# Kernel optimization log

Hardware: AMD Instinct MI355X
Metric: run time of the kernel (lower is better)

## Reference

```python
import jax, jax.numpy as jnp
import numpy as np

B, S, D = 4, 2048, 1024
H = 16
HD = D // H  # head dim = 64


def setup_inputs() -> dict:
    key = jax.random.key(0)
    ks = jax.random.split(key, 9)
    sc = 1.0 / np.sqrt(D)
    return {
        "x": jax.random.normal(ks[0], (B, S, D), jnp.float32),
        "Wq_w": jax.random.normal(ks[1], (D, D), jnp.float32) * sc,
        "Wq_b": jax.random.normal(ks[2], (D,), jnp.float32) * 0.01,
        "Wk_w": jax.random.normal(ks[3], (D, D), jnp.float32) * sc,
        "Wk_b": jax.random.normal(ks[4], (D,), jnp.float32) * 0.01,
        "Wv_w": jax.random.normal(ks[5], (D, D), jnp.float32) * sc,
        "Wv_b": jax.random.normal(ks[6], (D,), jnp.float32) * 0.01,
        "Wo_w": jax.random.normal(ks[7], (D, D), jnp.float32) * sc,
        "Wo_b": jax.random.normal(ks[8], (D,), jnp.float32) * 0.01,
    }


def reference(x, Wq_w, Wq_b, Wk_w, Wk_b, Wv_w, Wv_b, Wo_w, Wo_b):
    b, s, _ = x.shape
    # QKV projections (weights stored [in, out])
    q = x @ Wq_w + Wq_b
    k = x @ Wk_w + Wk_b
    v = x @ Wv_w + Wv_b
    # [b, s, D] -> [b, H, s, hd]
    q = q.reshape(b, s, H, HD).transpose(0, 2, 1, 3)
    k = k.reshape(b, s, H, HD).transpose(0, 2, 1, 3)
    v = v.reshape(b, s, H, HD).transpose(0, 2, 1, 3)
    # naive attention: full [b, H, s, s] scores, scale by head_dim**0.5
    scores = jnp.einsum("bhqd,bhkd->bhqk", q, k) / jnp.sqrt(jnp.float32(HD))
    # faithful to torch: tril(scores)==0 -> -inf (causal mask via tril of values)
    filt = jnp.tril(scores)
    scores = jnp.where(filt == 0, jnp.float32(-jnp.inf), scores)
    probs = jax.nn.softmax(scores, axis=-1)
    attn = jnp.einsum("bhqk,bhkd->bhqd", probs, v)
    # [b, H, s, hd] -> [b, s, D]
    attn = attn.transpose(0, 2, 1, 3).reshape(b, s, D)
    return attn @ Wo_w + Wo_b
```

## Files before the change

### kernel.cpp

```cpp
#include <hip/hip_runtime.h>
#include <hip/hip_bf16.h>


#define B_  4
#define S_  2048
#define D_  1024
#define H_  16
#define HD_ 64
#define M_  (B_*S_)
#define NT_ (S_/64)

typedef unsigned short u16;
typedef __attribute__((ext_vector_type(8))) short bf16x8;
typedef __attribute__((ext_vector_type(4))) float f32x4;
typedef __attribute__((ext_vector_type(8))) unsigned short ush8;
typedef __attribute__((ext_vector_type(4))) unsigned short ush4;

static __device__ __forceinline__ u16 f2b(float f) {
    unsigned int u = __float_as_uint(f);
    return (u16)((u + 0x7fffu + ((u >> 16) & 1u)) >> 16);
}

static __device__ __forceinline__ int cvt_pk_bf16(float a, float b) {
    int r;
    asm("v_cvt_pk_bf16_f32 %0, %1, %2" : "=v"(r) : "v"(a), "v"(b));
    return r;
}

#define EXP2(x) exp2f(x)

#define GLOAD_LDS16(g, l)                                                      \
    __builtin_amdgcn_global_load_lds(                                          \
        (const __attribute__((address_space(1))) void*)(g),                    \
        (__attribute__((address_space(3))) void*)(l), 16, 0, 0)

__global__ __launch_bounds__(256)
void cast_f32_bf16(const float* __restrict__ in, u16* __restrict__ out, int n8)
{
    int i = blockIdx.x * blockDim.x + threadIdx.x;
    const int stride = gridDim.x * blockDim.x;
    for (; i < n8; i += stride) {
        const float4 a = ((const float4*)in)[i*2+0];
        const float4 b = ((const float4*)in)[i*2+1];
        ush8 o;
        o[0]=f2b(a.x); o[1]=f2b(a.y); o[2]=f2b(a.z); o[3]=f2b(a.w);
        o[4]=f2b(b.x); o[5]=f2b(b.y); o[6]=f2b(b.z); o[7]=f2b(b.w);
        ((ush8*)out)[i] = o;
    }
}

__global__ __launch_bounds__(256)
void transpose_cast(const float* __restrict__ W, u16* __restrict__ Wt)
{
    __shared__ u16 T[64*72];
    const int tid = threadIdx.x;
    const int k0 = blockIdx.x * 64, n0 = blockIdx.y * 64;
    #pragma unroll
    for (int it = 0; it < 4; ++it) {
        const int li = tid + it*256;
        const int kk = li >> 4;
        const int nc = (li & 15) * 4;
        const float4 w4 = *(const float4*)&W[(size_t)(k0+kk)*D_ + n0 + nc];
        T[(nc+0)*72 + kk] = f2b(w4.x);
        T[(nc+1)*72 + kk] = f2b(w4.y);
        T[(nc+2)*72 + kk] = f2b(w4.z);
        T[(nc+3)*72 + kk] = f2b(w4.w);
    }
    __syncthreads();
    #pragma unroll
    for (int it = 0; it < 2; ++it) {
        const int li = tid + it*256;
        const int nr = li >> 3;
        const int kc = (li & 7) * 8;
        const ush8 v = *(const ush8*)&T[nr*72 + kc];
        *(ush8*)&Wt[(size_t)(n0+nr)*D_ + k0 + kc] = v;
    }
}

#define QSCALE 0.18033688f
#define TP_ 136

__global__ __launch_bounds__(256)
void gemm_qkv(const u16* __restrict__ A,
              const u16* __restrict__ wq, const u16* __restrict__ wk,
              const u16* __restrict__ wv,
              const float* __restrict__ bq, const float* __restrict__ bk,
              const float* __restrict__ bv,
              u16* __restrict__ oq, u16* __restrict__ ok, u16* __restrict__ ovt)
{
    __shared__ u16 sh[64*TP_];
    u16* As = sh;
    u16* Bs = sh + 4096;

    const int tid  = threadIdx.x;
    const int lane = tid & 63;
    const int wave = tid >> 6;
    const int wr = wave >> 1, wc = wave & 1;
    const int bm = blockIdx.x * 128;
    const int sel = blockIdx.y >> 3;
    const int bn = (blockIdx.y & 7) * 128;
    const u16* Bt = sel == 0 ? wq : sel == 1 ? wk : wv;
    const float* bias = sel == 0 ? bq : sel == 1 ? bk : bv;

    const int srow = wave*32 + (lane >> 2);
    const int sk   = (lane & 3) * 8;
    const u16* gA0 = A  + (size_t)(bm + srow)      * D_ + sk;
    const u16* gA1 = A  + (size_t)(bm + srow + 16) * D_ + sk;
    const u16* gB0 = Bt + (size_t)(bn + srow)      * D_ + sk;
    const u16* gB1 = Bt + (size_t)(bn + srow + 16) * D_ + sk;
    u16* lA0 = &As[(wave*2+0)*512];
    u16* lA1 = &As[(wave*2+1)*512];
    u16* lB0 = &Bs[(wave*2+0)*512];
    u16* lB1 = &Bs[(wave*2+1)*512];

    const f32x4 z4 = {0.f, 0.f, 0.f, 0.f};
    f32x4 acc[4][4];
    #pragma unroll
    for (int i = 0; i < 4; ++i)
        #pragma unroll
        for (int j = 0; j < 4; ++j) acc[i][j] = z4;

    const int cl = lane & 15;
    const int g  = lane >> 4;

    for (int k0 = 0; k0 < D_; k0 += 32) {
        GLOAD_LDS16(gA0 + k0, lA0);
        GLOAD_LDS16(gA1 + k0, lA1);
        GLOAD_LDS16(gB0 + k0, lB0);
        GLOAD_LDS16(gB1 + k0, lB1);
        __syncthreads();

        bf16x8 af[4], bfv[4];
        #pragma unroll
        for (int mf = 0; mf < 4; ++mf)
            af[mf] = *(const bf16x8*)&As[(wr*64 + mf*16 + cl)*32 + g*8];
        #pragma unroll
        for (int nf = 0; nf < 4; ++nf)
            bfv[nf] = *(const bf16x8*)&Bs[(wc*64 + nf*16 + cl)*32 + g*8];
        __builtin_amdgcn_s_setprio(1);
        #pragma unroll
        for (int mf = 0; mf < 4; ++mf)
            #pragma unroll
            for (int nf = 0; nf < 4; ++nf)
                acc[mf][nf] = __builtin_amdgcn_mfma_f32_16x16x32_bf16(
                    af[mf], bfv[nf], acc[mf][nf], 0, 0, 0);
        __builtin_amdgcn_s_setprio(0);
        __syncthreads();
    }

    if (sel == 2) {
        const int b = bm >> 11, s0 = bm & (S_-1);
        u16* T = sh;
        #pragma unroll
        for (int hh = 0; hh < 2; ++hh) {
            if (wc == hh) {
                #pragma unroll
                for (int nf = 0; nf < 4; ++nf) {
                    const float bvv = bias[bn + wc*64 + nf*16 + cl];
                    #pragma unroll
                    for (int mf = 0; mf < 4; ++mf) {
                        ush4 o4;
                        #pragma unroll
                        for (int r = 0; r < 4; ++r)
                            o4[r] = f2b(acc[mf][nf][r] + bvv);
                        *(ush4*)&T[(nf*16 + cl)*TP_ + wr*64 + mf*16 + g*4] = o4;
                    }
                }
            }
            __syncthreads();
            const int h = (bn >> 6) + hh;
            #pragma unroll
            for (int pp = 0; pp < 4; ++pp) {
                const int d = wave*16 + pp*4 + g;
                const ush8 vv = *(const ush8*)&T[d*TP_ + cl*8];
                *(ush8*)&ovt[((size_t)((b*H_ + h)*HD_ + d))*S_ + s0 + cl*8] = vv;
            }
            __syncthreads();
        }
    } else {
        const float oscale = sel == 0 ? QSCALE : 1.0f;
        u16* o = sel == 0 ? oq : ok;
        #pragma unroll
        for (int nf = 0; nf < 4; ++nf) {
            const int col = bn + wc*64 + nf*16 + cl;
            const float bvv = bias[col];
            const int h = col >> 6, d = col & (HD_-1);
            #pragma unroll
            for (int mf = 0; mf < 4; ++mf) {
                #pragma unroll
                for (int r = 0; r < 4; ++r) {
                    const int row = bm + wr*64 + mf*16 + g*4 + r;
                    const float v = (acc[mf][nf][r] + bvv) * oscale;
                    const int bb = row >> 11, s = row & (S_-1);
                    o[((size_t)(bb*H_ + h)*S_ + s)*HD_ + d] = f2b(v);
                }
            }
        }
    }
}

__global__ __launch_bounds__(256)
void gemm_oproj(const u16* __restrict__ A, const u16* __restrict__ Bt,
                const float* __restrict__ bias, float* __restrict__ out)
{
    __shared__ u16 As[128*32];
    __shared__ u16 Bs[128*32];
    const int tid  = threadIdx.x;
    const int lane = tid & 63;
    const int wave = tid >> 6;
    const int wr = wave >> 1, wc = wave & 1;
    const int bm = blockIdx.x * 128, bn = blockIdx.y * 128;

    const int srow = wave*32 + (lane >> 2);
    const int sk   = (lane & 3) * 8;
    const u16* gA0 = A  + (size_t)(bm + srow)      * D_ + sk;
    const u16* gA1 = A  + (size_t)(bm + srow + 16) * D_ + sk;
    const u16* gB0 = Bt + (size_t)(bn + srow)      * D_ + sk;
    const u16* gB1 = Bt + (size_t)(bn + srow + 16) * D_ + sk;
    u16* lA0 = &As[(wave*2+0)*512];
    u16* lA1 = &As[(wave*2+1)*512];
    u16* lB0 = &Bs[(wave*2+0)*512];
    u16* lB1 = &Bs[(wave*2+1)*512];

    const f32x4 z4 = {0.f, 0.f, 0.f, 0.f};
    f32x4 acc[4][4];
    #pragma unroll
    for (int i = 0; i < 4; ++i)
        #pragma unroll
        for (int j = 0; j < 4; ++j) acc[i][j] = z4;

    const int cl = lane & 15;
    const int g  = lane >> 4;

    for (int k0 = 0; k0 < D_; k0 += 32) {
        GLOAD_LDS16(gA0 + k0, lA0);
        GLOAD_LDS16(gA1 + k0, lA1);
        GLOAD_LDS16(gB0 + k0, lB0);
        GLOAD_LDS16(gB1 + k0, lB1);
        __syncthreads();

        bf16x8 af[4], bfv[4];
        #pragma unroll
        for (int mf = 0; mf < 4; ++mf)
            af[mf] = *(const bf16x8*)&As[(wr*64 + mf*16 + cl)*32 + g*8];
        #pragma unroll
        for (int nf = 0; nf < 4; ++nf)
            bfv[nf] = *(const bf16x8*)&Bs[(wc*64 + nf*16 + cl)*32 + g*8];
        __builtin_amdgcn_s_setprio(1);
        #pragma unroll
        for (int mf = 0; mf < 4; ++mf)
            #pragma unroll
            for (int nf = 0; nf < 4; ++nf)
                acc[mf][nf] = __builtin_amdgcn_mfma_f32_16x16x32_bf16(
                    af[mf], bfv[nf], acc[mf][nf], 0, 0, 0);
        __builtin_amdgcn_s_setprio(0);
        __syncthreads();
    }

    #pragma unroll
    for (int nf = 0; nf < 4; ++nf) {
        const int col = bn + wc*64 + nf*16 + cl;
        const float bvv = bias[col];
        #pragma unroll
        for (int mf = 0; mf < 4; ++mf) {
            #pragma unroll
            for (int r = 0; r < 4; ++r) {
                const int row = bm + wr*64 + mf*16 + g*4 + r;
                out[(size_t)row*D_ + col] = acc[mf][nf][r] + bvv;
            }
        }
    }
}

__global__ __launch_bounds__(256, 4)
void attn_bf16(const u16* __restrict__ Q, const u16* __restrict__ K,
               const u16* __restrict__ Vt, u16* __restrict__ out)
{
    __shared__ u16 Ks[2][64*64];
    __shared__ u16 Vs[2][64*64];

    const int tid  = threadIdx.x;
    const int lane = tid & 63;
    const int wave = tid >> 6;
    const int cl = lane & 15;
    const int g  = lane >> 4;
    const int swz = cl & 7;
    const int pair = blockIdx.x, h = blockIdx.y, b = blockIdx.z;
    const size_t base  = ((size_t)(b*H_ + h)) * S_ * HD_;
    const size_t vbase = ((size_t)(b*H_ + h)) * HD_ * S_;

    int qt = pair;
    const int n0 = pair + 1;

    const int r0 = tid >> 3;
    const int c0 = tid & 7;

    bf16x8 qf[2];
    #pragma unroll
    for (int ks = 0; ks < 2; ++ks)
        qf[ks] = *(const bf16x8*)&Q[base +
            (size_t)(qt*64 + wave*16 + cl)*HD_ + ks*32 + g*8];

    ush8 kreg[2], vreg[2];
    #pragma unroll
    for (int p = 0; p < 2; ++p) {
        kreg[p] = *(const ush8*)&K [base  + (size_t)(r0 + p*32)*HD_ + c0*8];
        vreg[p] = *(const ush8*)&Vt[vbase + (size_t)(r0 + p*32)*S_  + c0*8];
    }

    const f32x4 z4 = {0.f, 0.f, 0.f, 0.f};
    f32x4 oac[4];
    float m_i = -3.0e38f, l_i = 0.f;
    #pragma unroll
    for (int nf = 0; nf < 4; ++nf) oac[nf] = z4;

    int cur = 0;
    for (int t = 0; t < NT_ + 1; ++t) {
        const int kt = (t >= n0) ? t - n0 : t;

        if (t == n0) {
            const float inv = 1.f / l_i;
            const int srow = qt*64 + wave*16 + cl;
            #pragma unroll
            for (int nf = 0; nf < 4; ++nf) {
                ush4 o4;
                #pragma unroll
                for (int r = 0; r < 4; ++r) o4[r] = f2b(oac[nf][r] * inv);
                *(ush4*)&out[(size_t)(b*S_ + srow)*D_ + h*HD_ + nf*16 + g*4] = o4;
            }
            qt = NT_ - 1 - pair;
            #pragma unroll
            for (int ks = 0; ks < 2; ++ks)
                qf[ks] = *(const bf16x8*)&Q[base +
                    (size_t)(qt*64 + wave*16 + cl)*HD_ + ks*32 + g*8];
            m_i = -3.0e38f; l_i = 0.f;
            #pragma unroll
            for (int nf = 0; nf < 4; ++nf) oac[nf] = z4;
        }

        #pragma unroll
        for (int p = 0; p < 2; ++p) {
            const int row = r0 + p*32;
            const int slot = (c0 ^ (row & 7)) * 8;
            *(ush8*)&Ks[cur][row*64 + slot] = kreg[p];
            *(ush8*)&Vs[cur][row*64 + slot] = vreg[p];
        }
        __syncthreads();

        if (t + 1 < NT_ + 1) {
            const int nkt = (t + 1 >= n0) ? t + 1 - n0 : t + 1;
            #pragma unroll
            for (int p = 0; p < 2; ++p) {
                kreg[p] = *(const ush8*)&K [base  +
                    (size_t)(nkt*64 + r0 + p*32)*HD_ + c0*8];
                vreg[p] = *(const ush8*)&Vt[vbase +
                    (size_t)(r0 + p*32)*S_ + nkt*64 + c0*8];
            }
        }

        f32x4 sac[4];
        #pragma unroll
        for (int nf = 0; nf < 4; ++nf) sac[nf] = z4;
        __builtin_amdgcn_s_setprio(1);
        #pragma unroll
        for (int ks = 0; ks < 2; ++ks) {
            const int slot = ((ks*4 + g) ^ swz) * 8;
            #pragma unroll
            for (int nf = 0; nf < 4; ++nf) {
                const bf16x8 kf =
                    *(const bf16x8*)&Ks[cur][(nf*16 + cl)*64 + slot];
                sac[nf] = __builtin_amdgcn_mfma_f32_16x16x32_bf16(
                    kf, qf[ks], sac[nf], 0, 0, 0);
            }
        }
        __builtin_amdgcn_s_setprio(0);

        if (kt == qt) {
            const int qloc = wave*16 + cl;
            #pragma unroll
            for (int nf = 0; nf < 4; ++nf)
                #pragma unroll
                for (int r = 0; r < 4; ++r)
                    if (nf*16 + g*4 + r > qloc) sac[nf][r] = -3.0e38f;
        }

        float mx = -3.0e38f;
        #pragma unroll
        for (int nf = 0; nf < 4; ++nf)
            #pragma unroll
            for (int r = 0; r < 4; ++r) mx = fmaxf(mx, sac[nf][r]);
        mx = fmaxf(mx, __shfl_xor(mx, 16));
        mx = fmaxf(mx, __shfl_xor(mx, 32));
        const float mnew = fmaxf(m_i, mx);
        const float es = EXP2(m_i - mnew);
        float ls = 0.f;
        #pragma unroll
        for (int nf = 0; nf < 4; ++nf) {
            float s0 = EXP2(sac[nf][0] - mnew);
            float s1 = EXP2(sac[nf][1] - mnew);
            float s2 = EXP2(sac[nf][2] - mnew);
            float s3 = EXP2(sac[nf][3] - mnew);
            sac[nf][0] = s0; sac[nf][1] = s1; sac[nf][2] = s2; sac[nf][3] = s3;
            ls += (s0 + s1) + (s2 + s3);
        }
        ls += __shfl_xor(ls, 16);
        ls += __shfl_xor(ls, 32);
        m_i = mnew;
        l_i = l_i * es + ls;
        #pragma unroll
        for (int nf = 0; nf < 4; ++nf)
            #pragma unroll
            for (int r = 0; r < 4; ++r) oac[nf][r] *= es;

        int X[4], Y[4];
        #pragma unroll
        for (int nf = 0; nf < 4; ++nf) {
            X[nf] = cvt_pk_bf16(sac[nf][0], sac[nf][1]);
            Y[nf] = cvt_pk_bf16(sac[nf][2], sac[nf][3]);
        }

        const int sA = cl + ((g & 1) << 5);
        const bool hi = (g >> 1) != 0;
        __builtin_amdgcn_s_setprio(1);
        #pragma unroll
        for (int ks = 0; ks < 2; ++ks) {
            const int x0 = __shfl(X[2*ks],   sA);
            const int x1 = __shfl(X[2*ks+1], sA);
            const int y0 = __shfl(Y[2*ks],   sA);
            const int y1 = __shfl(Y[2*ks+1], sA);
            const int x2 = __shfl(X[2*ks],   sA + 16);
            const int x3 = __shfl(X[2*ks+1], sA + 16);
            const int y2 = __shfl(Y[2*ks],   sA + 16);
            const int y3 = __shfl(Y[2*ks+1], sA + 16);
            int4 w;
            w.x = hi ? x1 : x0;
            w.y = hi ? y1 : y0;
            w.z = hi ? x3 : x2;
            w.w = hi ? y3 : y2;
            const bf16x8 pb = __builtin_bit_cast(bf16x8, w);
            const int slot = ((ks*4 + g) ^ swz) * 8;
            #pragma unroll
            for (int nfd = 0; nfd < 4; ++nfd) {
                const bf16x8 vf =
                    *(const bf16x8*)&Vs[cur][(nfd*16 + cl)*64 + slot];
                oac[nfd] = __builtin_amdgcn_mfma_f32_16x16x32_bf16(
                    vf, pb, oac[nfd], 0, 0, 0);
            }
        }
        __builtin_amdgcn_s_setprio(0);
        cur ^= 1;
    }

    {
        const float inv = 1.f / l_i;
        const int srow = qt*64 + wave*16 + cl;
        #pragma unroll
        for (int nf = 0; nf < 4; ++nf) {
            ush4 o4;
            #pragma unroll
            for (int r = 0; r < 4; ++r) o4[r] = f2b(oac[nf][r] * inv);
            *(ush4*)&out[(size_t)(b*S_ + srow)*D_ + h*HD_ + nf*16 + g*4] = o4;
        }
    }
}

extern "C" void kernel_launch(void* const* d_in, const int* in_sizes, int n_in,
                              void* d_out, int out_size, void* d_ws, size_t ws_size,
                              hipStream_t stream)
{
    const float* x    = (const float*)d_in[0];
    const float* Wq_w = (const float*)d_in[1];
    const float* Wq_b = (const float*)d_in[2];
    const float* Wk_w = (const float*)d_in[3];
    const float* Wk_b = (const float*)d_in[4];
    const float* Wv_w = (const float*)d_in[5];
    const float* Wv_b = (const float*)d_in[6];
    const float* Wo_w = (const float*)d_in[7];
    const float* Wo_b = (const float*)d_in[8];
    float* out = (float*)d_out;

    u16* xb    = (u16*)d_ws;
    u16* wqt   = xb  + (size_t)M_*D_;
    u16* wkt   = wqt + (size_t)D_*D_;
    u16* wvt   = wkt + (size_t)D_*D_;
    u16* wot   = wvt + (size_t)D_*D_;
    u16* q     = wot + (size_t)D_*D_;
    u16* k     = q   + (size_t)M_*D_;
    u16* vt    = k   + (size_t)M_*D_;
    u16* attnb = vt  + (size_t)M_*D_;

    cast_f32_bf16<<<2048, 256, 0, stream>>>(x, xb, M_*D_/8);
    transpose_cast<<<dim3(16,16), 256, 0, stream>>>(Wq_w, wqt);
    transpose_cast<<<dim3(16,16), 256, 0, stream>>>(Wk_w, wkt);
    transpose_cast<<<dim3(16,16), 256, 0, stream>>>(Wv_w, wvt);
    transpose_cast<<<dim3(16,16), 256, 0, stream>>>(Wo_w, wot);

    gemm_qkv<<<dim3(M_/128, 24), 256, 0, stream>>>(
        xb, wqt, wkt, wvt, Wq_b, Wk_b, Wv_b, q, k, vt);

    attn_bf16<<<dim3(NT_/2, H_, B_), 256, 0, stream>>>(q, k, vt, attnb);

    gemm_oproj<<<dim3(M_/128, D_/128), 256, 0, stream>>>(attnb, wot, Wo_b, out);
}
```

Measured before the change: 299.0 us.

## Use 256x256 tiles with double-buffered swizzled LDS pipeline for projection GEMMs

Replaces the 128x128, 4-wave QKV and output-projection GEMMs with a shared 256x256-tile, 8-wave main loop. It uses K-step 64, XOR-swizzled LDS layout, and double buffering. The next tile's global-to-LDS loads are issued in the middle of MFMA phases. This raises arithmetic intensity per byte loaded, cuts LDS bank conflicts, and overlaps memory with compute. In exchange it uses far more LDS (about 128KB) and registers, which limits occupancy. The grid also shrinks: QKV gets 384 blocks, and O-proj only 128 blocks, which may underfill the GPU.

```diff
diff --git a/kernel.cpp b/kernel.cpp
--- a/kernel.cpp
+++ b/kernel.cpp
@@ -33,6 +33,8 @@
     __builtin_amdgcn_global_load_lds(                                          \
         (const __attribute__((address_space(1))) void*)(g),                    \
         (__attribute__((address_space(3))) void*)(l), 16, 0, 0)
+
+#define QSCALE 0.18033688f
 
 __global__ __launch_bounds__(256)
 void cast_f32_bf16(const float* __restrict__ in, u16* __restrict__ out, int n8)
@@ -77,196 +79,212 @@
     }
 }
 
-#define QSCALE 0.18033688f
-#define TP_ 136
-
-__global__ __launch_bounds__(256)
-void gemm_qkv(const u16* __restrict__ A,
-              const u16* __restrict__ wq, const u16* __restrict__ wk,
-              const u16* __restrict__ wv,
-              const float* __restrict__ bq, const float* __restrict__ bk,
-              const float* __restrict__ bv,
-              u16* __restrict__ oq, u16* __restrict__ ok, u16* __restrict__ ovt)
-{
-    __shared__ u16 sh[64*TP_];
-    u16* As = sh;
-    u16* Bs = sh + 4096;
-
+__device__ __forceinline__ void gemm256_loop(
+    const u16* __restrict__ Ag, size_t arow0,
+    const u16* __restrict__ Bg, size_t brow0,
+    u16* __restrict__ sh, f32x4 (&acc)[8][4])
+{
     const int tid  = threadIdx.x;
     const int lane = tid & 63;
     const int wave = tid >> 6;
-    const int wr = wave >> 1, wc = wave & 1;
-    const int bm = blockIdx.x * 128;
-    const int sel = blockIdx.y >> 3;
-    const int bn = (blockIdx.y & 7) * 128;
-    const u16* Bt = sel == 0 ? wq : sel == 1 ? wk : wv;
-    const float* bias = sel == 0 ? bq : sel == 1 ? bk : bv;
-
-    const int srow = wave*32 + (lane >> 2);
-    const int sk   = (lane & 3) * 8;
-    const u16* gA0 = A  + (size_t)(bm + srow)      * D_ + sk;
-    const u16* gA1 = A  + (size_t)(bm + srow + 16) * D_ + sk;
-    const u16* gB0 = Bt + (size_t)(bn + srow)      * D_ + sk;
-    const u16* gB1 = Bt + (size_t)(bn + srow + 16) * D_ + sk;
-    u16* lA0 = &As[(wave*2+0)*512];
-    u16* lA1 = &As[(wave*2+1)*512];
-    u16* lB0 = &Bs[(wave*2+0)*512];
-    u16* lB1 = &Bs[(wave*2+1)*512];
-
-    const f32x4 z4 = {0.f, 0.f, 0.f, 0.f};
-    f32x4 acc[4][4];
-    #pragma unroll
-    for (int i = 0; i < 4; ++i)
-        #pragma unroll
-        for (int j = 0; j < 4; ++j) acc[i][j] = z4;
-
-    const int cl = lane & 15;
-    const int g  = lane >> 4;
-
-    for (int k0 = 0; k0 < D_; k0 += 32) {
-        GLOAD_LDS16(gA0 + k0, lA0);
-        GLOAD_LDS16(gA1 + k0, lA1);
-        GLOAD_LDS16(gB0 + k0, lB0);
-        GLOAD_LDS16(gB1 + k0, lB1);
-        __syncthreads();
-
-        bf16x8 af[4], bfv[4];
-        #pragma unroll
-        for (int mf = 0; mf < 4; ++mf)
-            af[mf] = *(const bf16x8*)&As[(wr*64 + mf*16 + cl)*32 + g*8];
+    const int wr = wave >> 2, wc = wave & 3;
+    const int cl = lane & 15, g = lane >> 4;
+    const int sw = cl & 7;
+    u16* const Ab = sh;
+    u16* const Bb = sh + 32768;
+
+    const int srow   = lane >> 3;
+    const int schunk = (lane & 7) ^ srow;
+
+    auto stage_half = [&](const u16* gbase, size_t row0, int k0, u16* lbase) {
+        #pragma unroll
+        for (int i = 0; i < 2; ++i) {
+            const int seg = wave*2 + i;
+            const u16* src = gbase + (row0 + seg*8 + srow) * (size_t)D_
+                                   + k0 + schunk*8;
+            u16* dst = lbase + seg*512;
+            GLOAD_LDS16(src, dst);
+        }
+    };
+
+    stage_half(Ag, arow0,       0, Ab);
+    stage_half(Ag, arow0 + 128, 0, Ab + 8192);
+    stage_half(Bg, brow0,       0, Bb);
+    stage_half(Bg, brow0 + 128, 0, Bb + 8192);
+    __syncthreads();
+
+    for (int t = 0; t < 16; ++t) {
+        u16* const Ac = Ab + (t & 1) * 16384;
+        u16* const Bc = Bb + (t & 1) * 16384;
+        u16* const An = Ab + ((t + 1) & 1) * 16384;
+        u16* const Bn = Bb + ((t + 1) & 1) * 16384;
+        const int  kn   = (t + 1) * 64;
+        const bool more = (t < 15);
+
+        bf16x8 bfr[4][2];
         #pragma unroll
         for (int nf = 0; nf < 4; ++nf)
-            bfv[nf] = *(const bf16x8*)&Bs[(wc*64 + nf*16 + cl)*32 + g*8];
-        __builtin_amdgcn_s_setprio(1);
-        #pragma unroll
-        for (int mf = 0; mf < 4; ++mf)
-            #pragma unroll
-            for (int nf = 0; nf < 4; ++nf)
-                acc[mf][nf] = __builtin_amdgcn_mfma_f32_16x16x32_bf16(
-                    af[mf], bfv[nf], acc[mf][nf], 0, 0, 0);
-        __builtin_amdgcn_s_setprio(0);
-        __syncthreads();
-    }
-
-    if (sel == 2) {
-        const int b = bm >> 11, s0 = bm & (S_-1);
-        u16* T = sh;
-        #pragma unroll
-        for (int hh = 0; hh < 2; ++hh) {
-            if (wc == hh) {
+            #pragma unroll
+            for (int ks = 0; ks < 2; ++ks)
+                bfr[nf][ks] = *(const bf16x8*)
+                    &Bc[(wc*64 + nf*16 + cl)*64 + (((ks*4 + g) ^ sw) * 8)];
+
+        #pragma unroll
+        for (int p = 0; p < 4; ++p) {
+            bf16x8 af[2][2];
+            #pragma unroll
+            for (int e = 0; e < 2; ++e)
                 #pragma unroll
-                for (int nf = 0; nf < 4; ++nf) {
-                    const float bvv = bias[bn + wc*64 + nf*16 + cl];
+                for (int ks = 0; ks < 2; ++ks)
+                    af[e][ks] = *(const bf16x8*)
+                        &Ac[(wr*128 + (p*2 + e)*16 + cl)*64
+                            + (((ks*4 + g) ^ sw) * 8)];
+
+            if (p == 0 && more) {
+                stage_half(Ag, arow0,       kn, An);
+                stage_half(Ag, arow0 + 128, kn, An + 8192);
+            } else if (p == 1 && more) {
+                stage_half(Bg, brow0,       kn, Bn);
+                stage_half(Bg, brow0 + 128, kn, Bn + 8192);
+            }
+
+            __builtin_amdgcn_sched_barrier(0);
+            __builtin_amdgcn_s_barrier();
+            __builtin_amdgcn_sched_barrier(0);
+
+            __builtin_amdgcn_s_setprio(1);
+            #pragma unroll
+            for (int e = 0; e < 2; ++e)
+                #pragma unroll
+                for (int ks = 0; ks < 2; ++ks)
                     #pragma unroll
-                    for (int mf = 0; mf < 4; ++mf) {
-                        ush4 o4;
-                        #pragma unroll
-                        for (int r = 0; r < 4; ++r)
-                            o4[r] = f2b(acc[mf][nf][r] + bvv);
-                        *(ush4*)&T[(nf*16 + cl)*TP_ + wr*64 + mf*16 + g*4] = o4;
-                    }
-                }
-            }
-            __syncthreads();
-            const int h = (bn >> 6) + hh;
-            #pragma unroll
-            for (int pp = 0; pp < 4; ++pp) {
-                const int d = wave*16 + pp*4 + g;
-                const ush8 vv = *(const ush8*)&T[d*TP_ + cl*8];
-                *(ush8*)&ovt[((size_t)((b*H_ + h)*HD_ + d))*S_ + s0 + cl*8] = vv;
-            }
-            __syncthreads();
-        }
-    } else {
-        const float oscale = sel == 0 ? QSCALE : 1.0f;
-        u16* o = sel == 0 ? oq : ok;
-        #pragma unroll
-        for (int nf = 0; nf < 4; ++nf) {
-            const int col = bn + wc*64 + nf*16 + cl;
-            const float bvv = bias[col];
-            const int h = col >> 6, d = col & (HD_-1);
-            #pragma unroll
-            for (int mf = 0; mf < 4; ++mf) {
-                #pragma unroll
-                for (int r = 0; r < 4; ++r) {
-                    const int row = bm + wr*64 + mf*16 + g*4 + r;
-                    const float v = (acc[mf][nf][r] + bvv) * oscale;
-                    const int bb = row >> 11, s = row & (S_-1);
-                    o[((size_t)(bb*H_ + h)*S_ + s)*HD_ + d] = f2b(v);
-                }
-            }
-        }
-    }
-}
-
-__global__ __launch_bounds__(256)
-void gemm_oproj(const u16* __restrict__ A, const u16* __restrict__ Bt,
-                const float* __restrict__ bias, float* __restrict__ out)
-{
-    __shared__ u16 As[128*32];
-    __shared__ u16 Bs[128*32];
+                    for (int nf = 0; nf < 4; ++nf)
+                        acc[p*2 + e][nf] = __builtin_amdgcn_mfma_f32_16x16x32_bf16(
+                            af[e][ks], bfr[nf][ks], acc[p*2 + e][nf], 0, 0, 0);
+            __builtin_amdgcn_s_setprio(0);
+
+            if (p == 3) {
+                asm volatile("s_waitcnt vmcnt(0)" ::: "memory");
+            }
+            __builtin_amdgcn_sched_barrier(0);
+            __builtin_amdgcn_s_barrier();
+            __builtin_amdgcn_sched_barrier(0);
+        }
+    }
+    __syncthreads();
+}
+
+__global__ __launch_bounds__(512, 2)
+void gemm_qkv256(const u16* __restrict__ A,
+                 const u16* __restrict__ wq, const u16* __restrict__ wk,
+                 const u16* __restrict__ wv,
+                 const float* __restrict__ bq, const float* __restrict__ bk,
+                 const float* __restrict__ bv,
+                 u16* __restrict__ oq, u16* __restrict__ ok,
+                 u16* __restrict__ ovt)
+{
+    __shared__ u16 sh[67584];
+
     const int tid  = threadIdx.x;
     const int lane = tid & 63;
     const int wave = tid >> 6;
-    const int wr = wave >> 1, wc = wave & 1;
-    const int bm = blockIdx.x * 128, bn = blockIdx.y * 128;
-
-    const int srow = wave*32 + (lane >> 2);
-    const int sk   = (lane & 3) * 8;
-    const u16* gA0 = A  + (size_t)(bm + srow)      * D_ + sk;
-    const u16* gA1 = A  + (size_t)(bm + srow + 16) * D_ + sk;
-    const u16* gB0 = Bt + (size_t)(bn + srow)      * D_ + sk;
-    const u16* gB1 = Bt + (size_t)(bn + srow + 16) * D_ + sk;
-    u16* lA0 = &As[(wave*2+0)*512];
-    u16* lA1 = &As[(wave*2+1)*512];
-    u16* lB0 = &Bs[(wave*2+0)*512];
-    u16* lB1 = &Bs[(wave*2+1)*512];
-
+    const int wr = wave >> 2, wc = wave & 3;
+    const int cl = lane & 15, g = lane >> 4;
+    const size_t bm = (size_t)blockIdx.x * 256;
+    const int by   = blockIdx.y;
+    const int sel  = by >> 2;
+    const int bn2  = (by & 3) * 256;
+    const u16* Bt = sel == 0 ? wq : sel == 1 ? wk : wv;
+    const float* bias = sel == 0 ? bq : sel == 1 ? bk : bv;
+
+    f32x4 acc[8][4];
     const f32x4 z4 = {0.f, 0.f, 0.f, 0.f};
-    f32x4 acc[4][4];
-    #pragma unroll
-    for (int i = 0; i < 4; ++i)
+    #pragma unroll
+    for (int i = 0; i < 8; ++i)
         #pragma unroll
         for (int j = 0; j < 4; ++j) acc[i][j] = z4;
 
-    const int cl = lane & 15;
-    const int g  = lane >> 4;
-
-    for (int k0 = 0; k0 < D_; k0 += 32) {
-        GLOAD_LDS16(gA0 + k0, lA0);
-        GLOAD_LDS16(gA1 + k0, lA1);
-        GLOAD_LDS16(gB0 + k0, lB0);
-        GLOAD_LDS16(gB1 + k0, lB1);
+    gemm256_loop(A, bm, Bt, (size_t)bn2, sh, acc);
+
+    if (sel == 2) {
+        const int b  = (int)(bm >> 11);
+        const int s0 = (int)(bm & (S_ - 1));
+        #pragma unroll
+        for (int nf = 0; nf < 4; ++nf) {
+            const float bvv = bias[bn2 + wc*64 + nf*16 + cl];
+            #pragma unroll
+            for (int mf = 0; mf < 8; ++mf) {
+                ush4 o4;
+                #pragma unroll
+                for (int r = 0; r < 4; ++r) o4[r] = f2b(acc[mf][nf][r] + bvv);
+                *(ush4*)&sh[wc*16896 + (nf*16 + cl)*264 + wr*128 + mf*16 + g*4] = o4;
+            }
+        }
         __syncthreads();
-
-        bf16x8 af[4], bfv[4];
-        #pragma unroll
-        for (int mf = 0; mf < 4; ++mf)
-            af[mf] = *(const bf16x8*)&As[(wr*64 + mf*16 + cl)*32 + g*8];
-        #pragma unroll
-        for (int nf = 0; nf < 4; ++nf)
-            bfv[nf] = *(const bf16x8*)&Bs[(wc*64 + nf*16 + cl)*32 + g*8];
-        __builtin_amdgcn_s_setprio(1);
-        #pragma unroll
-        for (int mf = 0; mf < 4; ++mf)
-            #pragma unroll
-            for (int nf = 0; nf < 4; ++nf)
-                acc[mf][nf] = __builtin_amdgcn_mfma_f32_16x16x32_bf16(
-                    af[mf], bfv[nf], acc[mf][nf], 0, 0, 0);
-        __builtin_amdgcn_s_setprio(0);
-        __syncthreads();
-    }
+        const int head = wave >> 1, shalf = wave & 1;
+        const int hh = (bn2 >> 6) + head;
+        #pragma unroll
+        for (int it = 0; it < 16; ++it) {
+            const int lin = it*64 + lane;
+            const int d = lin >> 4, sc = lin & 15;
+            const ush8 vv = *(const ush8*)&sh[head*16896 + d*264 + shalf*128 + sc*8];
+            *(ush8*)&ovt[((size_t)((b*H_ + hh)*HD_ + d))*S_ + s0 + shalf*128 + sc*8] = vv;
+        }
+    } else {
+        const float osc = sel == 0 ? QSCALE : 1.0f;
+        u16* o = sel == 0 ? oq : ok;
+        #pragma unroll
+        for (int nf = 0; nf < 4; ++nf) {
+            const int col = bn2 + wc*64 + nf*16 + cl;
+            const float bvv = bias[col];
+            const int h = col >> 6, d = col & (HD_ - 1);
+            #pragma unroll
+            for (int mf = 0; mf < 8; ++mf) {
+                #pragma unroll
+                for (int r = 0; r < 4; ++r) {
+                    const size_t row = bm + wr*128 + mf*16 + g*4 + r;
+                    const int bb = (int)(row >> 11), s = (int)(row & (S_ - 1));
+                    o[((size_t)(bb*H_ + h)*S_ + s)*HD_ + d] =
+                        f2b((acc[mf][nf][r] + bvv) * osc);
+                }
+            }
+        }
+    }
+}
+
+__global__ __launch_bounds__(512, 2)
+void gemm_oproj256(const u16* __restrict__ A, const u16* __restrict__ Bt,
+                   const float* __restrict__ bias, float* __restrict__ out)
+{
+    __shared__ u16 sh[65536];
+
+    const int tid  = threadIdx.x;
+    const int lane = tid & 63;
+    const int wave = tid >> 6;
+    const int wr = wave >> 2, wc = wave & 3;
+    const int cl = lane & 15, g = lane >> 4;
+    const size_t bm = (size_t)blockIdx.x * 256;
+    const size_t bn = (size_t)blockIdx.y * 256;
+
+    f32x4 acc[8][4];
+    const f32x4 z4 = {0.f, 0.f, 0.f, 0.f};
+    #pragma unroll
+    for (int i = 0; i < 8; ++i)
+        #pragma unroll
+        for (int j = 0; j < 4; ++j) acc[i][j] = z4;
+
+    gemm256_loop(A, bm, Bt, bn, sh, acc);
 
     #pragma unroll
     for (int nf = 0; nf < 4; ++nf) {
-        const int col = bn + wc*64 + nf*16 + cl;
+        const int col = (int)bn + wc*64 + nf*16 + cl;
         const float bvv = bias[col];
         #pragma unroll
-        for (int mf = 0; mf < 4; ++mf) {
+        for (int mf = 0; mf < 8; ++mf) {
             #pragma unroll
             for (int r = 0; r < 4; ++r) {
-                const int row = bm + wr*64 + mf*16 + g*4 + r;
-                out[(size_t)row*D_ + col] = acc[mf][nf][r] + bvv;
+                const size_t row = bm + wr*128 + mf*16 + g*4 + r;
+                out[row*D_ + col] = acc[mf][nf][r] + bvv;
             }
         }
     }
@@ -495,10 +513,10 @@
     transpose_cast<<<dim3(16,16), 256, 0, stream>>>(Wv_w, wvt);
     transpose_cast<<<dim3(16,16), 256, 0, stream>>>(Wo_w, wot);
 
-    gemm_qkv<<<dim3(M_/128, 24), 256, 0, stream>>>(
+    gemm_qkv256<<<dim3(M_/256, 12), 512, 0, stream>>>(
         xb, wqt, wkt, wvt, Wq_b, Wk_b, Wv_b, q, k, vt);
 
     attn_bf16<<<dim3(NT_/2, H_, B_), 256, 0, stream>>>(q, k, vt, attnb);
 
-    gemm_oproj<<<dim3(M_/128, D_/128), 256, 0, stream>>>(attnb, wot, Wo_b, out);
-}
+    gemm_oproj256<<<dim3(M_/256, D_/256), 512, 0, stream>>>(attnb, wot, Wo_b, out);
+}
```

Result: no change. 293.7 us (-1.8%).
